# Kernel optimization log

Hardware: AMD Instinct MI355X
Metric: run time of the kernel (lower is better)

The kernel has to match this reference:

```python
import jax, jax.numpy as jnp
import numpy as np
from functools import partial

INPUT_DIM = 22
HIDDEN = 64
LAYERS = 3
OUT = 4
B, T = 1024, 512


def _lstm_layer(x_seq, w_ih, w_hh, b_ih, b_hh):
    # x_seq: [B, T, Din]; gate order (PyTorch): i, f, g, o
    Bsz = x_seq.shape[0]
    H = w_hh.shape[1]
    # precompute input projections for all timesteps: [B, T, 4H]
    x_proj = jnp.einsum('bti,gi->btg', x_seq, w_ih) + b_ih + b_hh

    def step(carry, xp):
        h, c = carry
        gates = xp + h @ w_hh.T  # [B, 4H]
        i, f, g, o = jnp.split(gates, 4, axis=-1)
        i = jax.nn.sigmoid(i)
        f = jax.nn.sigmoid(f)
        g = jnp.tanh(g)
        o = jax.nn.sigmoid(o)
        c = f * c + i * g
        h = o * jnp.tanh(c)
        return (h, c), h

    init = (jnp.zeros((Bsz, H), x_seq.dtype), jnp.zeros((Bsz, H), x_seq.dtype))
    _, hs = jax.lax.scan(step, init, jnp.swapaxes(x_proj, 0, 1))  # [T, B, H]
    return jnp.swapaxes(hs, 0, 1)  # [B, T, H]


def setup_inputs() -> dict:
    key = jax.random.key(0)
    ks = jax.random.split(key, 16)
    inp = {'x': jax.random.normal(ks[0], (B, INPUT_DIM, T), dtype=jnp.float32)}
    k = 1.0 / np.sqrt(HIDDEN)
    i = 1
    for l in range(LAYERS):
        din = INPUT_DIM if l == 0 else HIDDEN
        inp[f'w_ih{l}'] = jax.random.uniform(ks[i], (4 * HIDDEN, din), minval=-k, maxval=k); i += 1
        inp[f'w_hh{l}'] = jax.random.uniform(ks[i], (4 * HIDDEN, HIDDEN), minval=-k, maxval=k); i += 1
        inp[f'b_ih{l}'] = jax.random.uniform(ks[i], (4 * HIDDEN,), minval=-k, maxval=k); i += 1
        inp[f'b_hh{l}'] = jax.random.uniform(ks[i], (4 * HIDDEN,), minval=-k, maxval=k); i += 1
    inp['w_fc'] = jax.random.uniform(ks[i], (OUT, HIDDEN), minval=-k, maxval=k); i += 1
    inp['b_fc'] = jax.random.uniform(ks[i], (OUT,), minval=-k, maxval=k)
    return inp


def reference(x, w_ih0, w_hh0, b_ih0, b_hh0, w_ih1, w_hh1, b_ih1, b_hh1,
              w_ih2, w_hh2, b_ih2, b_hh2, w_fc, b_fc):
    # x: [B, 22, T] -> batch_first [B, T, 22]
    h = jnp.transpose(x, (0, 2, 1))
    h = _lstm_layer(h, w_ih0, w_hh0, b_ih0, b_hh0)
    # inter-layer dropout(0.4) is identity in eval/inference mode
    h = _lstm_layer(h, w_ih1, w_hh1, b_ih1, b_hh1)
    h = _lstm_layer(h, w_ih2, w_hh2, b_ih2, b_hh2)
    last = h[:, -1, :]  # [B, H]
    return last @ w_fc.T + b_fc  # [B, 4]
```

## Files before the change

kernel.cpp:

```cpp
#include <hip/hip_runtime.h>


#define TT   512
#define NTH  768
#define NBLK 256

typedef _Float16 h16;
typedef __attribute__((ext_vector_type(8))) _Float16 h16x8;
typedef __attribute__((ext_vector_type(4))) float f32x4;

#define MFMA16(a, b, c) __builtin_amdgcn_mfma_f32_16x16x32_f16((a), (b), (c), 0, 0, 0)

__device__ __forceinline__ float sigm(float z) {
    return __builtin_amdgcn_rcpf(1.f + __expf(-z));
}

__device__ __forceinline__ h16x8 loadB(const float* __restrict__ W, int ld, int ro,
                                       int k0, int kmax) {
    h16x8 r;
    #pragma unroll
    for (int i = 0; i < 8; ++i) {
        const int k = k0 + i;
        r[i] = (h16)((k < kmax) ? W[(size_t)ro * ld + k] : 0.f);
    }
    return r;
}

__global__ __attribute__((amdgpu_flat_work_group_size(NTH, NTH), amdgpu_waves_per_eu(3)))
void lstm_mfma(
    const float* __restrict__ x,
    const float* __restrict__ wih0, const float* __restrict__ whh0,
    const float* __restrict__ bih0, const float* __restrict__ bhh0,
    const float* __restrict__ wih1, const float* __restrict__ whh1,
    const float* __restrict__ bih1, const float* __restrict__ bhh1,
    const float* __restrict__ wih2, const float* __restrict__ whh2,
    const float* __restrict__ bih2, const float* __restrict__ bhh2,
    const float* __restrict__ wfc, const float* __restrict__ bfc,
    float* __restrict__ out)
{
    const int tid  = threadIdx.x;
    const int w    = tid >> 6;
    const int wl   = w >> 2;
    const int wg   = w & 3;
    const int lane = tid & 63;
    const int nloc = lane & 15;
    const int kg   = lane >> 4;
    const int b4   = blockIdx.x * 4;
    const int u    = wg * 16 + nloc;

    __shared__ alignas(16) h16 XL[2 * 32 * 512];
    __shared__ alignas(16) h16 HT[3 * 2 * 1024];
    __shared__ h16 PAD[3072];

    h16x8 Bf[4][4];
    float bias[4];
    #pragma unroll
    for (int g = 0; g < 4; ++g) {
        const int ro = g * 64 + u;
        if (wl == 0) {
            Bf[g][0] = loadB(wih0, 22, ro, kg * 8,      22);
            Bf[g][1] = loadB(whh0, 64, ro, kg * 8,      64);
            Bf[g][2] = loadB(whh0, 64, ro, 32 + kg * 8, 64);
            Bf[g][3] = Bf[g][2];
            bias[g]  = bih0[ro] + bhh0[ro];
        } else if (wl == 1) {
            Bf[g][0] = loadB(wih1, 64, ro, kg * 8,      64);
            Bf[g][1] = loadB(wih1, 64, ro, 32 + kg * 8, 64);
            Bf[g][2] = loadB(whh1, 64, ro, kg * 8,      64);
            Bf[g][3] = loadB(whh1, 64, ro, 32 + kg * 8, 64);
            bias[g]  = bih1[ro] + bhh1[ro];
        } else {
            Bf[g][0] = loadB(wih2, 64, ro, kg * 8,      64);
            Bf[g][1] = loadB(wih2, 64, ro, 32 + kg * 8, 64);
            Bf[g][2] = loadB(whh2, 64, ro, kg * 8,      64);
            Bf[g][3] = loadB(whh2, 64, ro, 32 + kg * 8, 64);
            bias[g]  = bih2[ro] + bhh2[ro];
        }
    }

    if (bias[0] > 1.0e30f) { PAD[tid & 2047] = (h16)bias[0]; out[0] = (float)PAD[0]; }

    {
        int* xz = (int*)XL;
        for (int i = tid; i < 2 * 32 * 256; i += NTH) xz[i] = 0;
        int* hz = (int*)HT;
        for (int i = tid; i < 3 * 2 * 512; i += NTH) hz[i] = 0;
    }
    __syncthreads();

    auto stage_x = [&](int chunk) {
        if (tid < 4 * 22) {
            const int bl = tid / 22, ii = tid - bl * 22;
            const float* src = x + (size_t)(b4 + bl) * (22 * 512) + (size_t)ii * 512
                                 + chunk * 32;
            h16* dst = &XL[(chunk & 1) * (32 * 512) + (ii >> 3) * 128 + (4 * bl) * 8 + (ii & 7)];
            #pragma unroll
            for (int q = 0; q < 8; ++q) {
                const float4 v = ((const float4*)src)[q];
                dst[(q * 4 + 0) * 512] = (h16)v.x;
                dst[(q * 4 + 1) * 512] = (h16)v.y;
                dst[(q * 4 + 2) * 512] = (h16)v.z;
                dst[(q * 4 + 3) * 512] = (h16)v.w;
            }
        }
    };
    stage_x(0);

    const int lo8  = lane * 8;
    const int hoff = (u >> 3) * 128 + kg * 32 + (u & 7);

    float cst = 0.f;

    auto ew = [&](const f32x4& zi, const f32x4& zf, const f32x4& zg, const f32x4& zo,
                  h16* hb) {
        const float vi = sigm(zi[0]);
        const float vf = sigm(zf[0]);
        const float vg = 2.f * sigm(2.f * zg[0]) - 1.f;
        const float vo = sigm(zo[0]);
        const float c  = vf * cst + vi * vg;
        cst = c;
        hb[hoff] = (h16)(vo * (2.f * sigm(2.f * c) - 1.f));
    };

    __syncthreads();

    #pragma unroll 1
    for (int t = 0; t < TT + 2; ++t) {
        const int wb = t & 1, rb = wb ^ 1;
        const h16* h0r = HT + 0 * 2048 + rb * 1024;
        h16*       h0w = HT + 0 * 2048 + wb * 1024;
        const h16* h1r = HT + 1 * 2048 + rb * 1024;
        h16*       h1w = HT + 1 * 2048 + wb * 1024;
        const h16* h2r = HT + 2 * 2048 + rb * 1024;
        h16*       h2w = HT + 2 * 2048 + wb * 1024;

        if (wl == 0) {
            if (t < TT) {
                const h16x8 ax   = *(const h16x8*)&XL[((t >> 5) & 1) * (32 * 512)
                                                      + (t & 31) * 512 + lo8];
                const h16x8 a0lo = *(const h16x8*)(h0r + lo8);
                const h16x8 a0hi = *(const h16x8*)(h0r + lo8 + 512);
                f32x4 z[4];
                #pragma unroll
                for (int g = 0; g < 4; ++g) {
                    z[g] = f32x4{bias[g], 0.f, 0.f, 0.f};
                    z[g] = MFMA16(ax,   Bf[g][0], z[g]);
                    z[g] = MFMA16(a0lo, Bf[g][1], z[g]);
                    z[g] = MFMA16(a0hi, Bf[g][2], z[g]);
                }
                ew(z[0], z[1], z[2], z[3], h0w);
            }
            if ((t & 31) == 16 && (t >> 5) < 15) stage_x((t >> 5) + 1);
        } else if (wl == 1) {
            if (t >= 1 && t < TT + 1) {
                const h16x8 a0lo = *(const h16x8*)(h0r + lo8);
                const h16x8 a0hi = *(const h16x8*)(h0r + lo8 + 512);
                const h16x8 a1lo = *(const h16x8*)(h1r + lo8);
                const h16x8 a1hi = *(const h16x8*)(h1r + lo8 + 512);
                f32x4 z[4];
                #pragma unroll
                for (int g = 0; g < 4; ++g) {
                    z[g] = f32x4{bias[g], 0.f, 0.f, 0.f};
                    z[g] = MFMA16(a0lo, Bf[g][0], z[g]);
                    z[g] = MFMA16(a0hi, Bf[g][1], z[g]);
                    z[g] = MFMA16(a1lo, Bf[g][2], z[g]);
                    z[g] = MFMA16(a1hi, Bf[g][3], z[g]);
                }
                ew(z[0], z[1], z[2], z[3], h1w);
            }
        } else {
            if (t >= 2) {
                const h16x8 a1lo = *(const h16x8*)(h1r + lo8);
                const h16x8 a1hi = *(const h16x8*)(h1r + lo8 + 512);
                const h16x8 a2lo = *(const h16x8*)(h2r + lo8);
                const h16x8 a2hi = *(const h16x8*)(h2r + lo8 + 512);
                f32x4 z[4];
                #pragma unroll
                for (int g = 0; g < 4; ++g) {
                    z[g] = f32x4{bias[g], 0.f, 0.f, 0.f};
                    z[g] = MFMA16(a1lo, Bf[g][0], z[g]);
                    z[g] = MFMA16(a1hi, Bf[g][1], z[g]);
                    z[g] = MFMA16(a2lo, Bf[g][2], z[g]);
                    z[g] = MFMA16(a2hi, Bf[g][3], z[g]);
                }
                ew(z[0], z[1], z[2], z[3], h2w);
            }
        }

        __syncthreads();
    }

    if (tid < 16) {
        const int ms = tid >> 2, o = tid & 3;
        const h16* h2 = HT + 2 * 2048 + 1024;
        float acc = bfc[o];
        #pragma unroll 1
        for (int uu = 0; uu < 64; ++uu)
            acc += (float)h2[(uu >> 3) * 128 + (4 * ms) * 8 + (uu & 7)] * wfc[o * 64 + uu];
        out[(b4 + ms) * 4 + o] = acc;
    }
}

extern "C" void kernel_launch(void* const* d_in, const int* in_sizes, int n_in,
                              void* d_out, int out_size, void* d_ws, size_t ws_size,
                              hipStream_t stream) {
    const float* x    = (const float*)d_in[0];
    const float* wih0 = (const float*)d_in[1];
    const float* whh0 = (const float*)d_in[2];
    const float* bih0 = (const float*)d_in[3];
    const float* bhh0 = (const float*)d_in[4];
    const float* wih1 = (const float*)d_in[5];
    const float* whh1 = (const float*)d_in[6];
    const float* bih1 = (const float*)d_in[7];
    const float* bhh1 = (const float*)d_in[8];
    const float* wih2 = (const float*)d_in[9];
    const float* whh2 = (const float*)d_in[10];
    const float* bih2 = (const float*)d_in[11];
    const float* bhh2 = (const float*)d_in[12];
    const float* wfc  = (const float*)d_in[13];
    const float* bfc  = (const float*)d_in[14];
    float* out = (float*)d_out;

    lstm_mfma<<<dim3(NBLK), dim3(NTH), 0, stream>>>(
        x, wih0, whh0, bih0, bhh0, wih1, whh1, bih1, bhh1,
        wih2, whh2, bih2, bhh2, wfc, bfc, out);
}
```

Baseline: 422.5 us.

## Precompute next-step input projections off the critical path and peel edge iterations

Each layer's wavefronts now compute the input-projection MFMAs for the following timestep after the elementwise update, so within a step only the recurrent MFMAs sit between the barrier and the h write. The pipeline deepens to two steps per layer (TT+4 ticks), and the timestep loop is split into prologue, steady-state and epilogue sections using compile-time edge flags to remove per-step bounds checks. This trades extra accumulator registers and a longer pipeline fill for a shorter dependency chain per barrier interval.

Result: faster. 395.8 us (-6.3%).

```diff
diff --git a/kernel.cpp b/kernel.cpp
--- a/kernel.cpp
+++ b/kernel.cpp
@@ -25,6 +25,9 @@
     }
     return r;
 }
+
+struct TrueC  { static constexpr bool value = true;  };
+struct FalseC { static constexpr bool value = false; };
 
 __global__ __attribute__((amdgpu_flat_work_group_size(NTH, NTH), amdgpu_waves_per_eu(3)))
 void lstm_mfma(
@@ -122,10 +125,24 @@
         hb[hoff] = (h16)(vo * (2.f * sigm(2.f * c) - 1.f));
     };
 
+    f32x4 zb[4];
+    #pragma unroll
+    for (int g = 0; g < 4; ++g) zb[g] = f32x4{bias[g], 0.f, 0.f, 0.f};
+
     __syncthreads();
 
-    #pragma unroll 1
-    for (int t = 0; t < TT + 2; ++t) {
+    f32x4 zc[4];
+    if (wl == 0) {
+        const h16x8 ax0 = *(const h16x8*)&XL[lo8];
+        #pragma unroll
+        for (int g = 0; g < 4; ++g) zc[g] = MFMA16(ax0, Bf[g][0], zb[g]);
+    } else {
+        #pragma unroll
+        for (int g = 0; g < 4; ++g) zc[g] = zb[g];
+    }
+
+    auto tick = [&](int t, auto edgec) {
+        constexpr bool EDGE = decltype(edgec)::value;
         const int wb = t & 1, rb = wb ^ 1;
         const h16* h0r = HT + 0 * 2048 + rb * 1024;
         h16*       h0w = HT + 0 * 2048 + wb * 1024;
@@ -135,60 +152,98 @@
         h16*       h2w = HT + 2 * 2048 + wb * 1024;
 
         if (wl == 0) {
-            if (t < TT) {
-                const h16x8 ax   = *(const h16x8*)&XL[((t >> 5) & 1) * (32 * 512)
-                                                      + (t & 31) * 512 + lo8];
-                const h16x8 a0lo = *(const h16x8*)(h0r + lo8);
-                const h16x8 a0hi = *(const h16x8*)(h0r + lo8 + 512);
-                f32x4 z[4];
-                #pragma unroll
-                for (int g = 0; g < 4; ++g) {
-                    z[g] = f32x4{bias[g], 0.f, 0.f, 0.f};
-                    z[g] = MFMA16(ax,   Bf[g][0], z[g]);
-                    z[g] = MFMA16(a0lo, Bf[g][1], z[g]);
+            const bool sa = !EDGE || (t < TT);
+            const bool ia = !EDGE || (t < TT - 1);
+            f32x4 z[4];
+            h16x8 a0lo, a0hi, axn;
+            if (sa) {
+                a0lo = *(const h16x8*)(h0r + lo8);
+                a0hi = *(const h16x8*)(h0r + lo8 + 512);
+            }
+            if (ia) {
+                const int tn = t + 1;
+                axn = *(const h16x8*)&XL[((tn >> 5) & 1) * (32 * 512) + (tn & 31) * 512 + lo8];
+            }
+            if (sa) {
+                #pragma unroll
+                for (int g = 0; g < 4; ++g) {
+                    z[g] = MFMA16(a0lo, Bf[g][1], zc[g]);
                     z[g] = MFMA16(a0hi, Bf[g][2], z[g]);
                 }
-                ew(z[0], z[1], z[2], z[3], h0w);
             }
             if ((t & 31) == 16 && (t >> 5) < 15) stage_x((t >> 5) + 1);
+            if (sa) ew(z[0], z[1], z[2], z[3], h0w);
+            if (ia) {
+                #pragma unroll
+                for (int g = 0; g < 4; ++g)
+                    zc[g] = MFMA16(axn, Bf[g][0], zb[g]);
+            }
         } else if (wl == 1) {
-            if (t >= 1 && t < TT + 1) {
-                const h16x8 a0lo = *(const h16x8*)(h0r + lo8);
-                const h16x8 a0hi = *(const h16x8*)(h0r + lo8 + 512);
-                const h16x8 a1lo = *(const h16x8*)(h1r + lo8);
-                const h16x8 a1hi = *(const h16x8*)(h1r + lo8 + 512);
-                f32x4 z[4];
-                #pragma unroll
-                for (int g = 0; g < 4; ++g) {
-                    z[g] = f32x4{bias[g], 0.f, 0.f, 0.f};
-                    z[g] = MFMA16(a0lo, Bf[g][0], z[g]);
-                    z[g] = MFMA16(a0hi, Bf[g][1], z[g]);
-                    z[g] = MFMA16(a1lo, Bf[g][2], z[g]);
+            const bool sa = !EDGE || (t >= 2 && t < TT + 2);
+            const bool ia = !EDGE || (t >= 1 && t < TT + 1);
+            f32x4 z[4];
+            h16x8 a1lo, a1hi, a0lo, a0hi;
+            if (sa) {
+                a1lo = *(const h16x8*)(h1r + lo8);
+                a1hi = *(const h16x8*)(h1r + lo8 + 512);
+            }
+            if (ia) {
+                a0lo = *(const h16x8*)(h0r + lo8);
+                a0hi = *(const h16x8*)(h0r + lo8 + 512);
+            }
+            if (sa) {
+                #pragma unroll
+                for (int g = 0; g < 4; ++g) {
+                    z[g] = MFMA16(a1lo, Bf[g][2], zc[g]);
                     z[g] = MFMA16(a1hi, Bf[g][3], z[g]);
                 }
-                ew(z[0], z[1], z[2], z[3], h1w);
+            }
+            if (sa) ew(z[0], z[1], z[2], z[3], h1w);
+            if (ia) {
+                #pragma unroll
+                for (int g = 0; g < 4; ++g) {
+                    f32x4 zn = MFMA16(a0lo, Bf[g][0], zb[g]);
+                    zc[g] = MFMA16(a0hi, Bf[g][1], zn);
+                }
             }
         } else {
-            if (t >= 2) {
-                const h16x8 a1lo = *(const h16x8*)(h1r + lo8);
-                const h16x8 a1hi = *(const h16x8*)(h1r + lo8 + 512);
-                const h16x8 a2lo = *(const h16x8*)(h2r + lo8);
-                const h16x8 a2hi = *(const h16x8*)(h2r + lo8 + 512);
-                f32x4 z[4];
-                #pragma unroll
-                for (int g = 0; g < 4; ++g) {
-                    z[g] = f32x4{bias[g], 0.f, 0.f, 0.f};
-                    z[g] = MFMA16(a1lo, Bf[g][0], z[g]);
-                    z[g] = MFMA16(a1hi, Bf[g][1], z[g]);
-                    z[g] = MFMA16(a2lo, Bf[g][2], z[g]);
+            const bool sa = !EDGE || (t >= 4);
+            const bool ia = !EDGE || (t >= 3 && t < TT + 3);
+            f32x4 z[4];
+            h16x8 a2lo, a2hi, a1lo, a1hi;
+            if (sa) {
+                a2lo = *(const h16x8*)(h2r + lo8);
+                a2hi = *(const h16x8*)(h2r + lo8 + 512);
+            }
+            if (ia) {
+                a1lo = *(const h16x8*)(h1r + lo8);
+                a1hi = *(const h16x8*)(h1r + lo8 + 512);
+            }
+            if (sa) {
+                #pragma unroll
+                for (int g = 0; g < 4; ++g) {
+                    z[g] = MFMA16(a2lo, Bf[g][2], zc[g]);
                     z[g] = MFMA16(a2hi, Bf[g][3], z[g]);
                 }
-                ew(z[0], z[1], z[2], z[3], h2w);
+            }
+            if (sa) ew(z[0], z[1], z[2], z[3], h2w);
+            if (ia) {
+                #pragma unroll
+                for (int g = 0; g < 4; ++g) {
+                    f32x4 zn = MFMA16(a1lo, Bf[g][0], zb[g]);
+                    zc[g] = MFMA16(a1hi, Bf[g][1], zn);
+                }
             }
         }
-
         __syncthreads();
-    }
+    };
+
+    #pragma unroll 1
+    for (int t = 0; t < 4; ++t) tick(t, TrueC{});
+    #pragma unroll 1
+    for (int t = 4; t < TT - 1; ++t) tick(t, FalseC{});
+    #pragma unroll 1
+    for (int t = TT - 1; t < TT + 4; ++t) tick(t, TrueC{});
 
     if (tid < 16) {
         const int ms = tid >> 2, o = tid & 3;
```
